# Optimization experiments

Measured on AMD Instinct MI355X. Metric: run time of the kernel, lower is better.

Reference implementation:

```python
import jax, jax.numpy as jnp
import numpy as np

N_NODES = 100000
N_EDGES = 1600000
IN_FEATS = 128
OUT_FEATS = 64


def setup_inputs() -> dict:
    key = jax.random.key(0)
    k1, k2, k3, k4 = jax.random.split(key, 4)
    feat = jax.random.normal(k1, (N_NODES, IN_FEATS), dtype=jnp.float32)
    W = jax.random.normal(k2, (IN_FEATS, OUT_FEATS), dtype=jnp.float32) * (1.0 / np.sqrt(IN_FEATS))
    src = jax.random.randint(k3, (N_EDGES,), 0, N_NODES, dtype=jnp.int64)
    dst = jax.random.randint(k4, (N_EDGES,), 0, N_NODES, dtype=jnp.int64)
    return {"feat": feat, "W": W, "src": src, "dst": dst}


def reference(feat, W, src, dst):
    # Linear projection (bias=False): homogeneous graph -> shared fc
    ft = feat @ W  # [N, out]

    # per-edge dot-product score: e_ij = <ft[src], ft[dst]>
    a = jnp.sum(ft[src] * ft[dst], axis=-1)  # [E]

    # edge softmax segmented by destination node (numerically stable)
    neg_inf = jnp.finfo(a.dtype).min
    m = jax.ops.segment_max(a, dst, num_segments=N_NODES)  # [N]
    m = jnp.where(m == neg_inf, 0.0, m)  # guard zero-in-degree nodes
    e = jnp.exp(a - m[dst])  # [E]
    s = jax.ops.segment_sum(e, dst, num_segments=N_NODES)  # [N]
    s = jnp.where(s == 0.0, 1.0, s)
    sa = e / s[dst]  # [E]

    # weighted scatter-sum aggregation: out[i] = sum_{j in N(i)} sa_ij * ft[j]
    rst = jax.ops.segment_sum(ft[src] * sa[:, None], dst, num_segments=N_NODES)
    return rst
```

## Files before the change

kernel.cpp:

```cpp
#include <hip/hip_runtime.h>
#include <hip/hip_fp16.h>
#include <math.h>

#define N_NODES 100000
#define N_EDGES 1600000
#define IN_F    128
#define OUT_F   64
#define K_BKT     196
#define BKT_SHIFT 9
#define BKT_NODES 512
#define BKT_CAP   10240
#define CHUNK     4096
#define PBLKS     ((N_EDGES + CHUNK - 1) / CHUNK)
#define LTILES    (N_NODES / 16)
#define LIN_BLKS  ((LTILES + 15) / 16)

typedef _Float16 half8 __attribute__((ext_vector_type(8)));
typedef float    f32x4 __attribute__((ext_vector_type(4)));


__global__ __launch_bounds__(1024) void partition_kernel(const int* __restrict__ src,
                                                         const int* __restrict__ dst,
                                                         int* __restrict__ bcursor,
                                                         unsigned* __restrict__ staging,
                                                         const float* __restrict__ W,
                                                         _Float16* __restrict__ WT) {
    __shared__ int hist[256], lbase[256], gbase[256], sc[256];
    __shared__ unsigned sval[CHUNK];
    __shared__ int spos[CHUNK];
    int t = threadIdx.x;
    if (blockIdx.x >= PBLKS) {
        if (t < 256) {
            int n = t & 63, kh = t >> 6;
            _Float16 tmp[32];
#pragma unroll
            for (int j = 0; j < 32; ++j)
                tmp[j] = (_Float16)W[(size_t)(kh * 32 + j) * OUT_F + n];
#pragma unroll
            for (int v = 0; v < 4; ++v)
                *(half8*)(WT + (size_t)n * IN_F + kh * 32 + v * 8) = *(half8*)&tmp[v * 8];
        }
        return;
    }
    if (t < 256) hist[t] = 0;
    __syncthreads();
    int beg = blockIdx.x * CHUNK;
    int end = min(beg + CHUNK, N_EDGES);
    for (int i = beg + t; i < end; i += 1024)
        atomicAdd(&hist[dst[i] >> BKT_SHIFT], 1);
    __syncthreads();
    if (t < 256) sc[t] = hist[t];
    __syncthreads();
    for (int off = 1; off < 256; off <<= 1) {
        int add = (t >= off && t < 256) ? sc[t - off] : 0;
        __syncthreads();
        if (t < 256) sc[t] += add;
        __syncthreads();
    }
    if (t < 256) {
        int v = hist[t];
        lbase[t] = sc[t] - v;
        if (t < K_BKT && v) gbase[t] = t * BKT_CAP + atomicAdd(&bcursor[t], v);
        hist[t] = 0;
    }
    __syncthreads();
    for (int i = beg + t; i < end; i += 1024) {
        int s = src[i], d = dst[i];
        int b = d >> BKT_SHIFT;
        int r = atomicAdd(&hist[b], 1);
        int lp = lbase[b] + r;
        sval[lp] = (unsigned)s | ((unsigned)(d & (BKT_NODES - 1)) << 17);
        spos[lp] = gbase[b] + r;
    }
    __syncthreads();
    int n = end - beg;
    for (int p = t; p < n; p += 1024) staging[spos[p]] = sval[p];
}

__global__ __launch_bounds__(1024) void place_linear_kernel(const unsigned* __restrict__ staging,
                                                            const int* __restrict__ bcursor,
                                                            int* __restrict__ row_beg,
                                                            int* __restrict__ row_end,
                                                            int* __restrict__ edge_src,
                                                            const float* __restrict__ feat,
                                                            const _Float16* __restrict__ WT,
                                                            __half* __restrict__ fth) {
    __shared__ int cnt[BKT_NODES], sc[BKT_NODES], lcur[BKT_NODES];
    int t = threadIdx.x;
    if (blockIdx.x < K_BKT) {
        if (t < BKT_NODES) cnt[t] = 0;
        __syncthreads();
        int base = blockIdx.x * BKT_CAP;
        int n = bcursor[blockIdx.x];
        for (int i = t; i < n; i += 1024)
            atomicAdd(&cnt[staging[base + i] >> 17], 1);
        __syncthreads();
        if (t < BKT_NODES) sc[t] = cnt[t];
        __syncthreads();
        for (int off = 1; off < BKT_NODES; off <<= 1) {
            int add = (t >= off && t < BKT_NODES) ? sc[t - off] : 0;
            __syncthreads();
            if (t < BKT_NODES) sc[t] += add;
            __syncthreads();
        }
        if (t < BKT_NODES) {
            int v = cnt[t];
            int b0 = base + sc[t] - v;
            lcur[t] = b0;
            int node = blockIdx.x * BKT_NODES + t;
            if (node < N_NODES) { row_beg[node] = b0; row_end[node] = b0 + v; }
        }
        __syncthreads();
        for (int i = base + t; i < base + n; i += 1024) {
            unsigned u = staging[i];
            int pos = atomicAdd(&lcur[u >> 17], 1);
            edge_src[pos] = (int)(u & 0x1FFFFu);
        }
        return;
    }
    int gwave = (blockIdx.x - K_BKT) * 16 + (t >> 6);
    if (gwave >= LTILES) return;
    int lane = t & 63;
    int m = lane & 15, kg = lane >> 4;
    int r0 = gwave * 16;

    half8 fb[4][4];
#pragma unroll
    for (int kb = 0; kb < 4; ++kb)
#pragma unroll
        for (int nb = 0; nb < 4; ++nb)
            fb[kb][nb] = *(const half8*)(WT + (size_t)(nb * 16 + m) * IN_F + kb * 32 + kg * 8);

    f32x4 acc[4];
#pragma unroll
    for (int nb = 0; nb < 4; ++nb) acc[nb] = (f32x4){0.f, 0.f, 0.f, 0.f};

#pragma unroll
    for (int kb = 0; kb < 4; ++kb) {
        const float4* ap = (const float4*)(feat + (size_t)(r0 + m) * IN_F + kb * 32 + kg * 8);
        float4 a0 = ap[0], a1 = ap[1];
        half8 fa = {(_Float16)a0.x, (_Float16)a0.y, (_Float16)a0.z, (_Float16)a0.w,
                    (_Float16)a1.x, (_Float16)a1.y, (_Float16)a1.z, (_Float16)a1.w};
#pragma unroll
        for (int nb = 0; nb < 4; ++nb)
            acc[nb] = __builtin_amdgcn_mfma_f32_16x16x32_f16(fa, fb[kb][nb], acc[nb], 0, 0, 0);
    }
#pragma unroll
    for (int nb = 0; nb < 4; ++nb)
#pragma unroll
        for (int i = 0; i < 4; ++i)
            fth[(size_t)(r0 + kg * 4 + i) * OUT_F + nb * 16 + m] = __float2half_rn(acc[nb][i]);
}

__global__ __launch_bounds__(256) void fused_node_kernel(const __half* __restrict__ fth,
                                                         const int* __restrict__ row_beg,
                                                         const int* __restrict__ row_end,
                                                         const int* __restrict__ edge_src,
                                                         float* __restrict__ out) {
    const float LOG2E = 1.44269504088896340736f;
    int wave = (blockIdx.x * 256 + threadIdx.x) >> 6;
    int lane = threadIdx.x & 63;
    if (wave >= N_NODES) return;
    int q = lane >> 4, ql = lane & 15;

    int beg = row_beg[wave];
    int end = row_end[wave];

    float2 rd = *(const float2*)(fth + (size_t)wave * OUT_F + 4 * ql);
    __half2 d01 = *(__half2*)&rd.x, d23 = *(__half2*)&rd.y;
    float fd0 = __half2float(d01.x) * LOG2E, fd1 = __half2float(d01.y) * LOG2E;
    float fd2 = __half2float(d23.x) * LOG2E, fd3 = __half2float(d23.y) * LOG2E;

    float m = -1e30f, l = 0.f;
    float a0 = 0.f, a1 = 0.f, a2 = 0.f, a3 = 0.f;

    for (int i = beg; i < end; i += 16) {
        int e0 = i + q, e1 = e0 + 4, e2 = e0 + 8, e3 = e0 + 12;
        bool u0 = e0 < end, u1 = e1 < end, u2 = e2 < end, u3 = e3 < end;
        int s0 = edge_src[u0 ? e0 : beg];
        int s1 = edge_src[u1 ? e1 : beg];
        int s2 = edge_src[u2 ? e2 : beg];
        int s3 = edge_src[u3 ? e3 : beg];
        float2 r0 = *(const float2*)(fth + (size_t)s0 * OUT_F + 4 * ql);
        float2 r1 = *(const float2*)(fth + (size_t)s1 * OUT_F + 4 * ql);
        float2 r2 = *(const float2*)(fth + (size_t)s2 * OUT_F + 4 * ql);
        float2 r3 = *(const float2*)(fth + (size_t)s3 * OUT_F + 4 * ql);
        __half2 A01 = *(__half2*)&r0.x, A23 = *(__half2*)&r0.y;
        __half2 B01 = *(__half2*)&r1.x, B23 = *(__half2*)&r1.y;
        __half2 C01 = *(__half2*)&r2.x, C23 = *(__half2*)&r2.y;
        __half2 D01 = *(__half2*)&r3.x, D23 = *(__half2*)&r3.y;
        float vA0 = __half2float(A01.x), vA1 = __half2float(A01.y);
        float vA2 = __half2float(A23.x), vA3 = __half2float(A23.y);
        float vB0 = __half2float(B01.x), vB1 = __half2float(B01.y);
        float vB2 = __half2float(B23.x), vB3 = __half2float(B23.y);
        float vC0 = __half2float(C01.x), vC1 = __half2float(C01.y);
        float vC2 = __half2float(C23.x), vC3 = __half2float(C23.y);
        float vD0 = __half2float(D01.x), vD1 = __half2float(D01.y);
        float vD2 = __half2float(D23.x), vD3 = __half2float(D23.y);

        float p0 = vA0 * fd0 + vA1 * fd1 + vA2 * fd2 + vA3 * fd3;
        float p1 = vB0 * fd0 + vB1 * fd1 + vB2 * fd2 + vB3 * fd3;
        float p2 = vC0 * fd0 + vC1 * fd1 + vC2 * fd2 + vC3 * fd3;
        float p3 = vD0 * fd0 + vD1 * fd1 + vD2 * fd2 + vD3 * fd3;
#pragma unroll
        for (int dd = 1; dd < 16; dd <<= 1) {
            p0 += __shfl_xor(p0, dd);
            p1 += __shfl_xor(p1, dd);
            p2 += __shfl_xor(p2, dd);
            p3 += __shfl_xor(p3, dd);
        }
        if (!u0) p0 = -1e30f;
        if (!u1) p1 = -1e30f;
        if (!u2) p2 = -1e30f;
        if (!u3) p3 = -1e30f;
        float nm = fmaxf(fmaxf(fmaxf(p0, p1), fmaxf(p2, p3)), m);
        float alpha = exp2f(m - nm);
        float w0 = exp2f(p0 - nm), w1 = exp2f(p1 - nm);
        float w2 = exp2f(p2 - nm), w3 = exp2f(p3 - nm);
        l = l * alpha + ((w0 + w1) + (w2 + w3));
        a0 = a0 * alpha + (w0 * vA0 + w1 * vB0) + (w2 * vC0 + w3 * vD0);
        a1 = a1 * alpha + (w0 * vA1 + w1 * vB1) + (w2 * vC1 + w3 * vD1);
        a2 = a2 * alpha + (w0 * vA2 + w1 * vB2) + (w2 * vC2 + w3 * vD2);
        a3 = a3 * alpha + (w0 * vA3 + w1 * vB3) + (w2 * vC3 + w3 * vD3);
        m = nm;
    }

#pragma unroll
    for (int dd = 16; dd <= 32; dd <<= 1) {
        float m2 = __shfl_xor(m, dd), l2 = __shfl_xor(l, dd);
        float b0 = __shfl_xor(a0, dd), b1 = __shfl_xor(a1, dd);
        float b2 = __shfl_xor(a2, dd), b3 = __shfl_xor(a3, dd);
        float M = fmaxf(m, m2);
        float e1 = exp2f(m - M), e2 = exp2f(m2 - M);
        l = l * e1 + l2 * e2;
        a0 = a0 * e1 + b0 * e2;
        a1 = a1 * e1 + b1 * e2;
        a2 = a2 * e1 + b2 * e2;
        a3 = a3 * e1 + b3 * e2;
        m = M;
    }
    if (q == 0) {
        float inv = (l > 0.f) ? 1.f / l : 0.f;
        *(float4*)(out + (size_t)wave * OUT_F + 4 * ql) =
            make_float4(a0 * inv, a1 * inv, a2 * inv, a3 * inv);
    }
}

extern "C" void kernel_launch(void* const* d_in, const int* in_sizes, int n_in,
                              void* d_out, int out_size, void* d_ws, size_t ws_size,
                              hipStream_t stream) {
    const float* feat = (const float*)d_in[0];
    const float* W    = (const float*)d_in[1];
    const int*   src  = (const int*)d_in[2];
    const int*   dst  = (const int*)d_in[3];
    float* out = (float*)d_out;

    __half*   fth      = (__half*)d_ws;
    unsigned* staging  = (unsigned*)((int*)d_ws + (size_t)N_NODES * OUT_F / 2);
    int*      edge_src = (int*)(staging + (size_t)K_BKT * BKT_CAP);
    int*      bcursor  = edge_src + (size_t)K_BKT * BKT_CAP;
    int*      row_beg  = bcursor + K_BKT;
    int*      row_end  = row_beg + N_NODES;
    _Float16* WT       = (_Float16*)(row_end + N_NODES);

    hipMemsetAsync(bcursor, 0, K_BKT * sizeof(int), stream);
    partition_kernel<<<PBLKS + 1, 1024, 0, stream>>>(src, dst, bcursor, staging, W, WT);
    place_linear_kernel<<<K_BKT + LIN_BLKS, 1024, 0, stream>>>(staging, bcursor, row_beg,
                                                               row_end, edge_src, feat, WT, fth);
    fused_node_kernel<<<(N_NODES * 64) / 256, 256, 0, stream>>>(fth, row_beg, row_end, edge_src, out);
}
```

Baseline: 205.5 us.

## Merge partition, linear and placement into one cooperative persistent kernel

Replaces the partition and place/linear kernels with a single persistent cooperative kernel of 256 blocks. It loops over edge chunks for bucket partitioning, then runs the MFMA projection, then does a grid-wide sync before per-bucket placement into CSR. The W transpose is dropped: each wave now reads W directly with strided loads and converts to half on the fly. This removes one kernel launch boundary and lets the projection overlap with partitioning in other blocks. The cost is cooperative-launch overhead, a grid barrier, and redundant per-wave W loads.

```diff
diff --git a/kernel.cpp b/kernel.cpp
--- a/kernel.cpp
+++ b/kernel.cpp
@@ -1,6 +1,9 @@
 #include <hip/hip_runtime.h>
+#include <hip/hip_cooperative_groups.h>
 #include <hip/hip_fp16.h>
 #include <math.h>
+
+namespace cg = cooperative_groups;
 
 #define N_NODES 100000
 #define N_EDGES 1600000
@@ -13,143 +16,141 @@
 #define CHUNK     4096
 #define PBLKS     ((N_EDGES + CHUNK - 1) / CHUNK)
 #define LTILES    (N_NODES / 16)
-#define LIN_BLKS  ((LTILES + 15) / 16)
+#define MEGA_BLKS 256
+#define MEGA_THR  1024
 
 typedef _Float16 half8 __attribute__((ext_vector_type(8)));
 typedef float    f32x4 __attribute__((ext_vector_type(4)));
 
 
-__global__ __launch_bounds__(1024) void partition_kernel(const int* __restrict__ src,
-                                                         const int* __restrict__ dst,
-                                                         int* __restrict__ bcursor,
-                                                         unsigned* __restrict__ staging,
-                                                         const float* __restrict__ W,
-                                                         _Float16* __restrict__ WT) {
+__global__ __launch_bounds__(MEGA_THR, 4) void mega_kernel(const int* __restrict__ src,
+                                                           const int* __restrict__ dst,
+                                                           int* __restrict__ bcursor,
+                                                           unsigned* __restrict__ staging,
+                                                           const float* __restrict__ feat,
+                                                           const float* __restrict__ W,
+                                                           __half* __restrict__ fth,
+                                                           int* __restrict__ row_beg,
+                                                           int* __restrict__ row_end,
+                                                           int* __restrict__ edge_src) {
     __shared__ int hist[256], lbase[256], gbase[256], sc[256];
     __shared__ unsigned sval[CHUNK];
     __shared__ int spos[CHUNK];
     int t = threadIdx.x;
-    if (blockIdx.x >= PBLKS) {
+
+    for (int c = blockIdx.x; c < PBLKS; c += MEGA_BLKS) {
+        if (t < 256) hist[t] = 0;
+        __syncthreads();
+        int beg = c * CHUNK;
+        int end = min(beg + CHUNK, N_EDGES);
+        for (int i = beg + t; i < end; i += MEGA_THR)
+            atomicAdd(&hist[dst[i] >> BKT_SHIFT], 1);
+        __syncthreads();
+        if (t < 256) sc[t] = hist[t];
+        __syncthreads();
+        for (int off = 1; off < 256; off <<= 1) {
+            int add = (t >= off && t < 256) ? sc[t - off] : 0;
+            __syncthreads();
+            if (t < 256) sc[t] += add;
+            __syncthreads();
+        }
         if (t < 256) {
-            int n = t & 63, kh = t >> 6;
-            _Float16 tmp[32];
-#pragma unroll
-            for (int j = 0; j < 32; ++j)
-                tmp[j] = (_Float16)W[(size_t)(kh * 32 + j) * OUT_F + n];
-#pragma unroll
-            for (int v = 0; v < 4; ++v)
-                *(half8*)(WT + (size_t)n * IN_F + kh * 32 + v * 8) = *(half8*)&tmp[v * 8];
-        }
-        return;
-    }
-    if (t < 256) hist[t] = 0;
-    __syncthreads();
-    int beg = blockIdx.x * CHUNK;
-    int end = min(beg + CHUNK, N_EDGES);
-    for (int i = beg + t; i < end; i += 1024)
-        atomicAdd(&hist[dst[i] >> BKT_SHIFT], 1);
-    __syncthreads();
-    if (t < 256) sc[t] = hist[t];
-    __syncthreads();
-    for (int off = 1; off < 256; off <<= 1) {
-        int add = (t >= off && t < 256) ? sc[t - off] : 0;
-        __syncthreads();
-        if (t < 256) sc[t] += add;
-        __syncthreads();
-    }
-    if (t < 256) {
-        int v = hist[t];
-        lbase[t] = sc[t] - v;
-        if (t < K_BKT && v) gbase[t] = t * BKT_CAP + atomicAdd(&bcursor[t], v);
-        hist[t] = 0;
-    }
-    __syncthreads();
-    for (int i = beg + t; i < end; i += 1024) {
-        int s = src[i], d = dst[i];
-        int b = d >> BKT_SHIFT;
-        int r = atomicAdd(&hist[b], 1);
-        int lp = lbase[b] + r;
-        sval[lp] = (unsigned)s | ((unsigned)(d & (BKT_NODES - 1)) << 17);
-        spos[lp] = gbase[b] + r;
-    }
-    __syncthreads();
-    int n = end - beg;
-    for (int p = t; p < n; p += 1024) staging[spos[p]] = sval[p];
-}
-
-__global__ __launch_bounds__(1024) void place_linear_kernel(const unsigned* __restrict__ staging,
-                                                            const int* __restrict__ bcursor,
-                                                            int* __restrict__ row_beg,
-                                                            int* __restrict__ row_end,
-                                                            int* __restrict__ edge_src,
-                                                            const float* __restrict__ feat,
-                                                            const _Float16* __restrict__ WT,
-                                                            __half* __restrict__ fth) {
-    __shared__ int cnt[BKT_NODES], sc[BKT_NODES], lcur[BKT_NODES];
-    int t = threadIdx.x;
-    if (blockIdx.x < K_BKT) {
-        if (t < BKT_NODES) cnt[t] = 0;
-        __syncthreads();
-        int base = blockIdx.x * BKT_CAP;
-        int n = bcursor[blockIdx.x];
-        for (int i = t; i < n; i += 1024)
-            atomicAdd(&cnt[staging[base + i] >> 17], 1);
-        __syncthreads();
-        if (t < BKT_NODES) sc[t] = cnt[t];
-        __syncthreads();
-        for (int off = 1; off < BKT_NODES; off <<= 1) {
-            int add = (t >= off && t < BKT_NODES) ? sc[t - off] : 0;
-            __syncthreads();
-            if (t < BKT_NODES) sc[t] += add;
-            __syncthreads();
-        }
-        if (t < BKT_NODES) {
-            int v = cnt[t];
-            int b0 = base + sc[t] - v;
-            lcur[t] = b0;
-            int node = blockIdx.x * BKT_NODES + t;
-            if (node < N_NODES) { row_beg[node] = b0; row_end[node] = b0 + v; }
-        }
-        __syncthreads();
-        for (int i = base + t; i < base + n; i += 1024) {
-            unsigned u = staging[i];
-            int pos = atomicAdd(&lcur[u >> 17], 1);
-            edge_src[pos] = (int)(u & 0x1FFFFu);
-        }
-        return;
-    }
-    int gwave = (blockIdx.x - K_BKT) * 16 + (t >> 6);
-    if (gwave >= LTILES) return;
-    int lane = t & 63;
-    int m = lane & 15, kg = lane >> 4;
-    int r0 = gwave * 16;
-
-    half8 fb[4][4];
-#pragma unroll
-    for (int kb = 0; kb < 4; ++kb)
-#pragma unroll
-        for (int nb = 0; nb < 4; ++nb)
-            fb[kb][nb] = *(const half8*)(WT + (size_t)(nb * 16 + m) * IN_F + kb * 32 + kg * 8);
-
-    f32x4 acc[4];
-#pragma unroll
-    for (int nb = 0; nb < 4; ++nb) acc[nb] = (f32x4){0.f, 0.f, 0.f, 0.f};
-
-#pragma unroll
-    for (int kb = 0; kb < 4; ++kb) {
-        const float4* ap = (const float4*)(feat + (size_t)(r0 + m) * IN_F + kb * 32 + kg * 8);
-        float4 a0 = ap[0], a1 = ap[1];
-        half8 fa = {(_Float16)a0.x, (_Float16)a0.y, (_Float16)a0.z, (_Float16)a0.w,
-                    (_Float16)a1.x, (_Float16)a1.y, (_Float16)a1.z, (_Float16)a1.w};
-#pragma unroll
-        for (int nb = 0; nb < 4; ++nb)
-            acc[nb] = __builtin_amdgcn_mfma_f32_16x16x32_f16(fa, fb[kb][nb], acc[nb], 0, 0, 0);
-    }
-#pragma unroll
-    for (int nb = 0; nb < 4; ++nb)
-#pragma unroll
-        for (int i = 0; i < 4; ++i)
-            fth[(size_t)(r0 + kg * 4 + i) * OUT_F + nb * 16 + m] = __float2half_rn(acc[nb][i]);
+            int v = hist[t];
+            lbase[t] = sc[t] - v;
+            if (t < K_BKT && v) gbase[t] = t * BKT_CAP + atomicAdd(&bcursor[t], v);
+            hist[t] = 0;
+        }
+        __syncthreads();
+        for (int i = beg + t; i < end; i += MEGA_THR) {
+            int s = src[i], d = dst[i];
+            int b = d >> BKT_SHIFT;
+            int r = atomicAdd(&hist[b], 1);
+            int lp = lbase[b] + r;
+            sval[lp] = (unsigned)s | ((unsigned)(d & (BKT_NODES - 1)) << 17);
+            spos[lp] = gbase[b] + r;
+        }
+        __syncthreads();
+        int n = end - beg;
+        for (int p = t; p < n; p += MEGA_THR) staging[spos[p]] = sval[p];
+        __syncthreads();
+    }
+
+    {
+        int lane = t & 63;
+        int m = lane & 15, kg = lane >> 4;
+        int nw = MEGA_BLKS * (MEGA_THR / 64);
+        for (int gwave = blockIdx.x * (MEGA_THR / 64) + (t >> 6); gwave < LTILES; gwave += nw) {
+            int r0 = gwave * 16;
+            half8 fb[4][4];
+#pragma unroll
+            for (int kb = 0; kb < 4; ++kb)
+#pragma unroll
+                for (int nb = 0; nb < 4; ++nb) {
+                    const float* wp = W + (size_t)(kb * 32 + kg * 8) * OUT_F + nb * 16 + m;
+#pragma unroll
+                    for (int j = 0; j < 8; ++j)
+                        fb[kb][nb][j] = (_Float16)wp[j * OUT_F];
+                }
+            f32x4 acc[4];
+#pragma unroll
+            for (int nb = 0; nb < 4; ++nb) acc[nb] = (f32x4){0.f, 0.f, 0.f, 0.f};
+#pragma unroll
+            for (int kb = 0; kb < 4; ++kb) {
+                const float4* ap = (const float4*)(feat + (size_t)(r0 + m) * IN_F + kb * 32 + kg * 8);
+                float4 a0 = ap[0], a1 = ap[1];
+                half8 fa = {(_Float16)a0.x, (_Float16)a0.y, (_Float16)a0.z, (_Float16)a0.w,
+                            (_Float16)a1.x, (_Float16)a1.y, (_Float16)a1.z, (_Float16)a1.w};
+#pragma unroll
+                for (int nb = 0; nb < 4; ++nb)
+                    acc[nb] = __builtin_amdgcn_mfma_f32_16x16x32_f16(fa, fb[kb][nb], acc[nb], 0, 0, 0);
+            }
+#pragma unroll
+            for (int nb = 0; nb < 4; ++nb)
+#pragma unroll
+                for (int i = 0; i < 4; ++i)
+                    fth[(size_t)(r0 + kg * 4 + i) * OUT_F + nb * 16 + m] = __float2half_rn(acc[nb][i]);
+        }
+    }
+
+    __threadfence();
+    cg::this_grid().sync();
+
+    {
+        int* cnt  = spos;
+        int* psc  = spos + BKT_NODES;
+        int* lcur = spos + 2 * BKT_NODES;
+        for (int b = blockIdx.x; b < K_BKT; b += MEGA_BLKS) {
+            if (t < BKT_NODES) cnt[t] = 0;
+            __syncthreads();
+            int base = b * BKT_CAP;
+            int n = bcursor[b];
+            for (int i = t; i < n; i += MEGA_THR)
+                atomicAdd(&cnt[staging[base + i] >> 17], 1);
+            __syncthreads();
+            if (t < BKT_NODES) psc[t] = cnt[t];
+            __syncthreads();
+            for (int off = 1; off < BKT_NODES; off <<= 1) {
+                int add = (t >= off && t < BKT_NODES) ? psc[t - off] : 0;
+                __syncthreads();
+                if (t < BKT_NODES) psc[t] += add;
+                __syncthreads();
+            }
+            if (t < BKT_NODES) {
+                int v = cnt[t];
+                int b0 = base + psc[t] - v;
+                lcur[t] = b0;
+                int node = b * BKT_NODES + t;
+                if (node < N_NODES) { row_beg[node] = b0; row_end[node] = b0 + v; }
+            }
+            __syncthreads();
+            for (int i = base + t; i < base + n; i += MEGA_THR) {
+                unsigned u = staging[i];
+                int pos = atomicAdd(&lcur[u >> 17], 1);
+                edge_src[pos] = (int)(u & 0x1FFFFu);
+            }
+            __syncthreads();
+        }
+    }
 }
 
 __global__ __launch_bounds__(256) void fused_node_kernel(const __half* __restrict__ fth,
@@ -261,11 +262,12 @@
     int*      bcursor  = edge_src + (size_t)K_BKT * BKT_CAP;
     int*      row_beg  = bcursor + K_BKT;
     int*      row_end  = row_beg + N_NODES;
-    _Float16* WT       = (_Float16*)(row_end + N_NODES);
-
-    hipMemsetAsync(bcursor, 0, K_BKT * sizeof(int), stream);
-    partition_kernel<<<PBLKS + 1, 1024, 0, stream>>>(src, dst, bcursor, staging, W, WT);
-    place_linear_kernel<<<K_BKT + LIN_BLKS, 1024, 0, stream>>>(staging, bcursor, row_beg,
-                                                               row_end, edge_src, feat, WT, fth);
+
+    (void)hipMemsetAsync(bcursor, 0, K_BKT * sizeof(int), stream);
+    void* kargs[] = {(void*)&src, (void*)&dst, (void*)&bcursor, (void*)&staging,
+                     (void*)&feat, (void*)&W, (void*)&fth,
+                     (void*)&row_beg, (void*)&row_end, (void*)&edge_src};
+    (void)hipLaunchCooperativeKernel((const void*)mega_kernel, dim3(MEGA_BLKS), dim3(MEGA_THR),
+                                     kargs, 0, stream);
     fused_node_kernel<<<(N_NODES * 64) / 256, 256, 0, stream>>>(fth, row_beg, row_end, edge_src, out);
 }
```

New measurement: 388.5 us. +89.1%, slower.
